# Performance work log

Measured on AMD Instinct MI355X. Metric: run time of the kernel, lower is better.

## Reference

```python
import jax, jax.numpy as jnp
import numpy as np

EPS = 1e-5
NUM_SUBSET = 3

def conv1x1(x, w, b):
    # x: (N,C,T,V), w: (O,C), b: (O,)
    return jnp.einsum('nctv,oc->notv', x, w) + b[None, :, None, None]

def batchnorm(x, w, b):
    m = x.mean(axis=(0, 2, 3), keepdims=True)
    v = x.var(axis=(0, 2, 3), keepdims=True)
    return (x - m) * jax.lax.rsqrt(v + EPS) * w[None, :, None, None] + b[None, :, None, None]

def setup_inputs() -> dict:
    key = jax.random.key(0)
    ks = jax.random.split(key, 16)
    N, C, T, V, R, O, S = 32, 64, 256, 25, 8, 64, NUM_SUBSET
    sc = 0.05
    return {
        'x1': jax.random.normal(ks[0], (N, C, T, V), jnp.float32),
        'x2': jax.random.normal(ks[1], (N, C, T, V), jnp.float32),
        'PA': jax.random.normal(ks[2], (S, V, V), jnp.float32) * sc,
        'alpha': jnp.zeros((1,), jnp.float32),
        'c1w': jax.random.normal(ks[3], (S, R, C), jnp.float32) * sc,
        'c1b': jnp.zeros((S, R), jnp.float32),
        'c2w': jax.random.normal(ks[4], (S, R, C), jnp.float32) * sc,
        'c2b': jnp.zeros((S, R), jnp.float32),
        'c3w': jax.random.normal(ks[5], (S, O, C), jnp.float32) * sc,
        'c3b': jnp.zeros((S, O), jnp.float32),
        'c4w': jax.random.normal(ks[6], (S, O, C), jnp.float32) * sc,
        'c4b': jnp.zeros((S, O), jnp.float32),
        'c5w': jax.random.normal(ks[7], (S, O, R), jnp.float32) * sc,
        'c5b': jnp.zeros((S, O), jnp.float32),
        'c6w': jax.random.normal(ks[8], (S, O, R), jnp.float32) * sc,
        'c6b': jnp.zeros((S, O), jnp.float32),
        'bn1_w': jax.random.uniform(ks[9], (O,), jnp.float32),
        'bn1_b': jnp.zeros((O,), jnp.float32),
        'bn2_w': jax.random.uniform(ks[10], (O,), jnp.float32),
        'bn2_b': jnp.zeros((O,), jnp.float32),
    }

def reference(x1, x2, PA, alpha, c1w, c1b, c2w, c2b, c3w, c3b, c4w, c4b,
              c5w, c5b, c6w, c6b, bn1_w, bn1_b, bn2_w, bn2_b):
    y1 = y2 = None
    for i in range(NUM_SUBSET):
        r1 = conv1x1(x1, c1w[i], c1b[i]).mean(axis=2)  # (N,R,V)
        r2 = conv1x1(x2, c2w[i], c2b[i]).mean(axis=2)  # (N,R,V)
        x3 = conv1x1(x1, c3w[i], c3b[i])               # (N,O,T,V)
        x4 = conv1x1(x2, c4w[i], c4b[i])               # (N,O,T,V)
        rel = jnp.tanh(r1[:, :, :, None] - r2[:, :, None, :])  # (N,R,V,V)
        # NOTE: source passes self.alpha (scalar param) into the A2 slot,
        # so the `alpha` multiplier on conv5 defaults to 1.
        a1 = jnp.einsum('nruv,or->nouv', rel, c5w[i]) + c5b[i][None, :, None, None]
        a1 = a1 + PA[i][None, None, :, :]
        a2 = jnp.einsum('nruv,or->nouv', rel, c6w[i]) + c6b[i][None, :, None, None] + alpha
        z1 = jnp.einsum('ncuv,nctv->nctu', a1, x3)
        z2 = jnp.einsum('ncuv,nctv->nctu', a2, x4)
        y1 = z1 if y1 is None else y1 + z1
        y2 = z2 if y2 is None else y2 + z2
    # in_channels == out_channels -> residual down is identity
    y1 = jax.nn.relu(batchnorm(y1, bn1_w, bn1_b) + x1)
    y2 = jax.nn.relu(batchnorm(y2, bn2_w, bn2_b) + x2)
    return (y1, y2)
```

## Files before the change

### kernel.cpp

```cpp
#include <hip/hip_runtime.h>

typedef float  f32x4  __attribute__((ext_vector_type(4)));
typedef short  bf16x8 __attribute__((ext_vector_type(8)));
typedef short  s16x4  __attribute__((ext_vector_type(4)));

__device__ __forceinline__ unsigned short f2bf(float f) {
    unsigned int u = __float_as_uint(f);
    unsigned int r = (u + 0x7FFFu + ((u >> 16) & 1u)) >> 16;
    return (unsigned short)r;
}
__device__ __forceinline__ float bf2f(unsigned short h) {
    return __uint_as_float(((unsigned int)h) << 16);
}

__global__ __launch_bounds__(256) void kT_transpose(
    const float* __restrict__ x1, const float* __restrict__ x2,
    float* __restrict__ xm, unsigned short* __restrict__ xT)
{
    const int tc = blockIdx.x, n = blockIdx.y, p = blockIdx.z;
    const float* __restrict__ x = p ? x2 : x1;
    __shared__ unsigned short tile[64 * 225];
    const int tid = threadIdx.x;

    const size_t xb = (size_t)n * 409600 + (size_t)tc * 200;
    for (int k = 0; k < 13; k++) {
        const int idx = tid + k * 256;
        if (idx < 3200) {
            const int c = idx / 50, l = idx % 50;
            const f32x4 v = *(const f32x4*)(x + xb + (size_t)c * 6400 + l * 4);
            const int base = c * 225 + l * 4;
            tile[base + 0] = f2bf(v[0]);
            tile[base + 1] = f2bf(v[1]);
            tile[base + 2] = f2bf(v[2]);
            tile[base + 3] = f2bf(v[3]);
        }
    }
    __syncthreads();

    for (int k = 0; k < 7; k++) {
        const int idx = tid + k * 256;
        if (idx < 1600) {
            const int c = idx / 25, v = idx % 25;
            float s = 0.f;
            #pragma unroll
            for (int t = 0; t < 8; t++) s += bf2f(tile[c * 225 + t * 25 + v]);
            atomicAdd(&xm[((size_t)(p * 32 + n) * 64 + c) * 25 + v],
                      s * (1.0f / 256.0f));
        }
    }

    for (int k = 0; k < 7; k++) {
        const int idx = tid + k * 256;
        if (idx < 1600) {
            const int c8 = idx & 7, pos = idx >> 3;
            bf16x8 o;
            #pragma unroll
            for (int j = 0; j < 8; j++)
                o[j] = (short)tile[(c8 * 8 + j) * 225 + pos];
            *(bf16x8*)(xT + (((size_t)(p * 32 + n) * 6400 + tc * 200 + pos) * 64
                             + c8 * 8)) = o;
        }
    }
}

__global__ void k2_adj(const float* __restrict__ xm,
                       const float* __restrict__ PA, const float* __restrict__ alpha,
                       const float* __restrict__ c1w, const float* __restrict__ c1b,
                       const float* __restrict__ c2w, const float* __restrict__ c2b,
                       const float* __restrict__ c5w, const float* __restrict__ c5b,
                       const float* __restrict__ c6w, const float* __restrict__ c6b,
                       unsigned short* __restrict__ aw,
                       const float* __restrict__ c3w, const float* __restrict__ c4w,
                       unsigned short* __restrict__ awW)
{
    const int b = blockIdx.x;
    const int tid = threadIdx.x;

    if (b >= 192) {
        const int pi = b - 192;
        const int p = pi / 3, i = pi % 3;
        const int cg = tid >> 6, lane = tid & 63, q = lane >> 4, m = lane & 15;
        const float* w3 = p ? c4w : c3w;
        const float* wr = w3 + (size_t)(i * 64 + cg * 16 + m) * 64 + q * 8;
        const f32x4 w00 = *(const f32x4*)(wr);
        const f32x4 w01 = *(const f32x4*)(wr + 4);
        const f32x4 w10 = *(const f32x4*)(wr + 32);
        const f32x4 w11 = *(const f32x4*)(wr + 36);
        bf16x8 af0, af1;
        #pragma unroll
        for (int k = 0; k < 4; k++) {
            af0[k] = (short)f2bf(w00[k]); af0[k + 4] = (short)f2bf(w01[k]);
            af1[k] = (short)f2bf(w10[k]); af1[k + 4] = (short)f2bf(w11[k]);
        }
        unsigned short* o = awW + ((size_t)(pi * 4 + cg) * 64 + lane) * 16;
        *(bf16x8*)(o)     = af0;
        *(bf16x8*)(o + 8) = af1;
        return;
    }

    const int i = b >> 6;
    const int n = (b >> 1) & 31;
    const int pp = b & 1;
    __shared__ float xml[3200];
    __shared__ float rl[400];
    __shared__ float rel[5000];

    for (int idx = tid; idx < 3200; idx += 256) {
        const int p_ = idx / 1600, rest = idx % 1600;
        xml[idx] = xm[(size_t)(p_ * 32 + n) * 1600 + rest];
    }
    __syncthreads();

    for (int idx = tid; idx < 400; idx += 256) {
        const int which = idx / 200;
        const int rr = (idx % 200) / 25;
        const int v = idx % 25;
        const float* wv = (which ? c2w : c1w) + (i * 8 + rr) * 64;
        const float* xp = xml + which * 1600;
        float s = (which ? c2b : c1b)[i * 8 + rr];
        for (int c = 0; c < 64; c++) s += wv[c] * xp[c * 25 + v];
        rl[idx] = s;
    }
    __syncthreads();

    for (int idx = tid; idx < 5000; idx += 256) {
        const int r_ = idx / 625;
        const int rem = idx - r_ * 625;
        const int u = rem / 25;
        const int v = rem - u * 25;
        rel[idx] = tanhf(rl[r_ * 25 + u] - rl[200 + r_ * 25 + v]);
    }
    __syncthreads();

    const float al = alpha[0];
    {
        const int p_ = pp;
        const float* w5 = p_ ? c6w : c5w;
        const float* b5 = p_ ? c6b : c5b;
        for (int idx = tid; idx < 8192; idx += 256) {
            const int c = idx >> 7;
            const int ut = (idx >> 6) & 1;
            const int lane = idx & 63;
            const int u = ut * 16 + (lane & 15);
            const int qd = lane >> 4;
            bf16x8 outv;
            if (u < 25) {
                float wrow[8];
                #pragma unroll
                for (int r = 0; r < 8; r++) wrow[r] = w5[(i * 64 + c) * 8 + r];
                const float bias = b5[i * 64 + c];
                #pragma unroll
                for (int j = 0; j < 8; j++) {
                    const int v = qd * 8 + j;
                    float s = 0.f;
                    if (v < 25) {
                        s = bias + (p_ ? al : PA[i * 625 + u * 25 + v]);
                        #pragma unroll
                        for (int r = 0; r < 8; r++) s += rel[r * 625 + u * 25 + v] * wrow[r];
                    }
                    outv[j] = (short)f2bf(s);
                }
            } else {
                #pragma unroll
                for (int j = 0; j < 8; j++) outv[j] = 0;
            }
            *(bf16x8*)(aw + ((size_t)((p_ * 3 + i) * 32 + n) * 64 + c) * 1024
                          + ut * 512 + lane * 8) = outv;
        }
    }
}

__global__ __launch_bounds__(256, 3) void kF_main(
    const unsigned short* __restrict__ xT,
    const float* __restrict__ c3b, const float* __restrict__ c4b,
    const unsigned short* __restrict__ awW,
    const unsigned short* __restrict__ aw,
    unsigned short* __restrict__ z,
    float* __restrict__ ppart)
{
    const int flat = blockIdx.x;
    const int lidx = flat >> 3;
    const int grp  = (flat & 7) * 8 + (lidx >> 6);
    const int within = lidx & 63;
    const int tc = within & 15, cg = within >> 4;
    const int n = grp & 31, p = grp >> 5;

    __shared__ unsigned short X3s[2][16 * 512];
    const int tid = threadIdx.x, w = tid >> 6, lane = tid & 63;
    const int q = lane >> 4, m = lane & 15;

    {
        int* xi = (int*)&X3s[0][0];
        #pragma unroll
        for (int k = 0; k < 32; k++) xi[tid + k * 256] = 0;
    }

    const float* __restrict__ b3 = p ? c4b : c3b;
    const size_t xTb = ((size_t)(p * 32 + n) * 6400 + (size_t)tc * 400) * 64;

    bf16x8 xr0[7], xr1[7];
    #pragma unroll
    for (int k = 0; k < 7; k++) {
        const int g = w + 4 * k;
        if (g < 25) {
            const unsigned short* xp = xT + xTb + (size_t)(g * 16 + m) * 64 + q * 8;
            xr0[k] = *(const bf16x8*)(xp);
            xr1[k] = *(const bf16x8*)(xp + 32);
        }
    }

    f32x4 acc[4][2];
    #pragma unroll
    for (int a = 0; a < 4; a++) {
        acc[a][0] = (f32x4){0.f, 0.f, 0.f, 0.f};
        acc[a][1] = (f32x4){0.f, 0.f, 0.f, 0.f};
    }

    __syncthreads();

    for (int i = 0; i < 3; i++) {
        bf16x8 B0[4], B1[4];
        #pragma unroll
        for (int cl4 = 0; cl4 < 4; cl4++) {
            const int c = cg * 16 + w * 4 + cl4;
            const unsigned short* ab =
                aw + ((size_t)((p * 3 + i) * 32 + n) * 64 + c) * 1024 + lane * 8;
            B0[cl4] = *(const bf16x8*)(ab);
            B1[cl4] = *(const bf16x8*)(ab + 512);
        }

        const unsigned short* wp =
            awW + ((size_t)((p * 3 + i) * 4 + cg) * 64 + lane) * 16;
        const bf16x8 af0 = *(const bf16x8*)(wp);
        const bf16x8 af1 = *(const bf16x8*)(wp + 8);
        float bb[4];
        #pragma unroll
        for (int r = 0; r < 4; r++) bb[r] = b3[i * 64 + cg * 16 + q * 4 + r];

        unsigned short* Xb = &X3s[i & 1][0];
        #pragma unroll
        for (int k = 0; k < 7; k++) {
            const int g = w + 4 * k;
            if (g < 25) {
                f32x4 d = (f32x4){0.f, 0.f, 0.f, 0.f};
                d = __builtin_amdgcn_mfma_f32_16x16x32_bf16(af0, xr0[k], d, 0, 0, 0);
                d = __builtin_amdgcn_mfma_f32_16x16x32_bf16(af1, xr1[k], d, 0, 0, 0);
                const int pos = g * 16 + m;
                const int t = pos / 25, v = pos - t * 25;
                #pragma unroll
                for (int r = 0; r < 4; r++)
                    Xb[(q * 4 + r) * 512 + t * 32 + v] = f2bf(d[r] + bb[r]);
            }
        }
        __syncthreads();

        #pragma unroll
        for (int cl4 = 0; cl4 < 4; cl4++) {
            const int cl = w * 4 + cl4;
            const bf16x8 A = *(const bf16x8*)(Xb + cl * 512 + m * 32 + q * 8);
            acc[cl4][0] = __builtin_amdgcn_mfma_f32_16x16x32_bf16(A, B0[cl4], acc[cl4][0], 0, 0, 0);
            acc[cl4][1] = __builtin_amdgcn_mfma_f32_16x16x32_bf16(A, B1[cl4], acc[cl4][1], 0, 0, 0);
        }
    }
    __syncthreads();

    unsigned short* stg = &X3s[0][0];
    #pragma unroll
    for (int cl4 = 0; cl4 < 4; cl4++) {
        float sum = 0.f, ssq = 0.f;
        #pragma unroll
        for (int r = 0; r < 4; r++) {
            const float v0 = acc[cl4][0][r];
            sum += v0; ssq += v0 * v0;
        }
        if (m < 9) {
            #pragma unroll
            for (int r = 0; r < 4; r++) {
                const float v1 = acc[cl4][1][r];
                sum += v1; ssq += v1 * v1;
            }
        }
        #pragma unroll
        for (int off = 32; off > 0; off >>= 1) {
            sum += __shfl_xor(sum, off, 64);
            ssq += __shfl_xor(ssq, off, 64);
        }
        const int c = cg * 16 + w * 4 + cl4;
        if (lane == 0) {
            float* pp = ppart + ((size_t)(p * 64 + c) * 512 + n * 16 + tc) * 2;
            pp[0] = sum; pp[1] = ssq;
        }
        #pragma unroll
        for (int ut = 0; ut < 2; ut++) {
            if (ut == 0 || m < 9) {
                #pragma unroll
                for (int r = 0; r < 4; r++)
                    stg[w * 1600 + cl4 * 400 + (q * 4 + r) * 25 + ut * 16 + m] =
                        f2bf(acc[cl4][ut][r]);
            }
        }
    }
    for (int rd = 0; rd < 4; rd++) {
        const int idx = rd * 64 + lane;
        if (idx < 200) {
            const int cl4 = idx / 50, oct = idx % 50;
            const bf16x8 vz = *(const bf16x8*)(stg + w * 1600 + cl4 * 400 + oct * 8);
            const int c = cg * 16 + w * 4 + cl4;
            *(bf16x8*)(z + ((size_t)((p * 32 + n) * 64 + c)) * 6400
                         + tc * 400 + oct * 8) = vz;
        }
    }
}

__global__ void k4_finalize(const float* __restrict__ ppart,
                            const float* __restrict__ bn1w, const float* __restrict__ bn1b,
                            const float* __restrict__ bn2w, const float* __restrict__ bn2b,
                            float* __restrict__ ss)
{
    const int b = blockIdx.x;
    const int t = threadIdx.x;
    const float* base = ppart + (size_t)b * 1024;
    float s = 0.f, qs = 0.f;
    #pragma unroll
    for (int k = 0; k < 8; k++) {
        const int idx = t + 64 * k;
        s  += base[idx * 2];
        qs += base[idx * 2 + 1];
    }
    #pragma unroll
    for (int off = 32; off > 0; off >>= 1) {
        s  += __shfl_xor(s,  off, 64);
        qs += __shfl_xor(qs, off, 64);
    }
    if (t == 0) {
        const int p = b >> 6, c = b & 63;
        const float cnt = 204800.f;
        const float mean = s / cnt;
        const float var  = qs / cnt - mean * mean;
        const float gw = p ? bn2w[c] : bn1w[c];
        const float gb = p ? bn2b[c] : bn1b[c];
        const float scale = gw * rsqrtf(var + 1e-5f);
        ss[b * 2]     = scale;
        ss[b * 2 + 1] = gb - mean * scale;
    }
}

__global__ __launch_bounds__(256) void k5_apply(
    const float* __restrict__ x1, const float* __restrict__ x2,
    const unsigned short* __restrict__ z, const float* __restrict__ ss,
    float* __restrict__ out)
{
    const unsigned int g = blockIdx.x * 256u + threadIdx.x;
    const unsigned int e = g * 4u;
    const int p = (e >= 13107200u) ? 1 : 0;
    const unsigned int c = (e / 6400u) & 63u;
    const float* xsrc = p ? x2 : x1;
    const f32x4 xv = *(const f32x4*)(xsrc + (e - (unsigned int)p * 13107200u));
    const s16x4 zv = *(const s16x4*)(const void*)(z + e);
    const float scale = ss[(p * 64 + c) * 2];
    const float shift = ss[(p * 64 + c) * 2 + 1];
    f32x4 o;
    #pragma unroll
    for (int k = 0; k < 4; k++) {
        const float zf = bf2f((unsigned short)zv[k]);
        const float y = zf * scale + shift + xv[k];
        o[k] = y > 0.f ? y : 0.f;
    }
    *(f32x4*)(out + e) = o;
}

extern "C" void kernel_launch(void* const* d_in, const int* in_sizes, int n_in,
                              void* d_out, int out_size, void* d_ws, size_t ws_size,
                              hipStream_t stream)
{
    (void)in_sizes; (void)n_in; (void)out_size; (void)ws_size;
    const float* x1   = (const float*)d_in[0];
    const float* x2   = (const float*)d_in[1];
    const float* PA   = (const float*)d_in[2];
    const float* alp  = (const float*)d_in[3];
    const float* c1w  = (const float*)d_in[4];
    const float* c1b  = (const float*)d_in[5];
    const float* c2w  = (const float*)d_in[6];
    const float* c2b  = (const float*)d_in[7];
    const float* c3w  = (const float*)d_in[8];
    const float* c3b  = (const float*)d_in[9];
    const float* c4w  = (const float*)d_in[10];
    const float* c4b  = (const float*)d_in[11];
    const float* c5w  = (const float*)d_in[12];
    const float* c5b  = (const float*)d_in[13];
    const float* c6w  = (const float*)d_in[14];
    const float* c6b  = (const float*)d_in[15];
    const float* bn1w = (const float*)d_in[16];
    const float* bn1b = (const float*)d_in[17];
    const float* bn2w = (const float*)d_in[18];
    const float* bn2b = (const float*)d_in[19];

    char* ws = (char*)d_ws;
    float*          xm    = (float*)(ws + 0);
    unsigned short* aw    = (unsigned short*)(ws + 409600);
    unsigned short* xT    = (unsigned short*)(ws + 25575424);
    unsigned short* zbuf  = (unsigned short*)(ws + 78004224);
    float*          ppart = (float*)(ws + 130433024);
    float*          ss    = (float*)(ws + 130957312);
    unsigned short* awW   = (unsigned short*)(ws + 130958336);

    hipMemsetAsync(xm, 0, 409600, stream);

    kT_transpose<<<dim3(32, 32, 2), 256, 0, stream>>>(x1, x2, xm, xT);
    k2_adj<<<198, 256, 0, stream>>>(xm, PA, alp, c1w, c1b, c2w, c2b,
                                    c5w, c5b, c6w, c6b, aw, c3w, c4w, awW);
    kF_main<<<dim3(4096), 256, 0, stream>>>(xT, c3b, c4b, awW, aw,
                                            zbuf, ppart);
    k4_finalize<<<128, 64, 0, stream>>>(ppart, bn1w, bn1b, bn2w, bn2b, ss);
    k5_apply<<<25600, 256, 0, stream>>>(x1, x2, zbuf, ss, (float*)d_out);
}
```

Baseline: 373.8 us.

## Pipeline kF stages with swizzled LDS, replace atomics with partial means

Several changes at once. The time-mean now goes to per-tile partial buffers that k2 sums, replacing the atomics and the memset. kF_main is software-pipelined so stage-1 MFMA for subset i+1 overlaps stage-2 for subset i, with one fewer barrier per iteration. LDS tiles get an XOR swizzle and padding to cut bank conflicts. Float-to-bf16 conversion uses the packed hip intrinsic. This adds register pressure in kF and extra reads in k2, and the partial buffer aliases zbuf.

```diff
diff --git a/kernel.cpp b/kernel.cpp
--- a/kernel.cpp
+++ b/kernel.cpp
@@ -1,13 +1,17 @@
 #include <hip/hip_runtime.h>
+#include <hip/hip_bf16.h>
 
 typedef float  f32x4  __attribute__((ext_vector_type(4)));
 typedef short  bf16x8 __attribute__((ext_vector_type(8)));
 typedef short  s16x4  __attribute__((ext_vector_type(4)));
 
 __device__ __forceinline__ unsigned short f2bf(float f) {
-    unsigned int u = __float_as_uint(f);
-    unsigned int r = (u + 0x7FFFu + ((u >> 16) & 1u)) >> 16;
-    return (unsigned short)r;
+    __hip_bfloat16 h = __float2bfloat16(f);
+    return *reinterpret_cast<unsigned short*>(&h);
+}
+__device__ __forceinline__ unsigned int f2bf2(float a, float b) {
+    __hip_bfloat162 h = __float22bfloat162_rn(make_float2(a, b));
+    return *reinterpret_cast<unsigned int*>(&h);
 }
 __device__ __forceinline__ float bf2f(unsigned short h) {
     return __uint_as_float(((unsigned int)h) << 16);
@@ -15,11 +19,11 @@
 
 __global__ __launch_bounds__(256) void kT_transpose(
     const float* __restrict__ x1, const float* __restrict__ x2,
-    float* __restrict__ xm, unsigned short* __restrict__ xT)
+    float* __restrict__ xmp, unsigned short* __restrict__ xT)
 {
     const int tc = blockIdx.x, n = blockIdx.y, p = blockIdx.z;
     const float* __restrict__ x = p ? x2 : x1;
-    __shared__ unsigned short tile[64 * 225];
+    __shared__ unsigned short tile[64 * 226];
     const int tid = threadIdx.x;
 
     const size_t xb = (size_t)n * 409600 + (size_t)tc * 200;
@@ -28,11 +32,9 @@
         if (idx < 3200) {
             const int c = idx / 50, l = idx % 50;
             const f32x4 v = *(const f32x4*)(x + xb + (size_t)c * 6400 + l * 4);
-            const int base = c * 225 + l * 4;
-            tile[base + 0] = f2bf(v[0]);
-            tile[base + 1] = f2bf(v[1]);
-            tile[base + 2] = f2bf(v[2]);
-            tile[base + 3] = f2bf(v[3]);
+            unsigned int* dst = (unsigned int*)&tile[c * 226 + l * 4];
+            dst[0] = f2bf2(v[0], v[1]);
+            dst[1] = f2bf2(v[2], v[3]);
         }
     }
     __syncthreads();
@@ -43,9 +45,9 @@
             const int c = idx / 25, v = idx % 25;
             float s = 0.f;
             #pragma unroll
-            for (int t = 0; t < 8; t++) s += bf2f(tile[c * 225 + t * 25 + v]);
-            atomicAdd(&xm[((size_t)(p * 32 + n) * 64 + c) * 25 + v],
-                      s * (1.0f / 256.0f));
+            for (int t = 0; t < 8; t++) s += bf2f(tile[c * 226 + t * 25 + v]);
+            xmp[((size_t)((p * 32 + n) * 32 + tc)) * 1600 + idx] =
+                s * (1.0f / 256.0f);
         }
     }
 
@@ -56,14 +58,14 @@
             bf16x8 o;
             #pragma unroll
             for (int j = 0; j < 8; j++)
-                o[j] = (short)tile[(c8 * 8 + j) * 225 + pos];
+                o[j] = (short)tile[(c8 * 8 + j) * 226 + pos];
             *(bf16x8*)(xT + (((size_t)(p * 32 + n) * 6400 + tc * 200 + pos) * 64
                              + c8 * 8)) = o;
         }
     }
 }
 
-__global__ void k2_adj(const float* __restrict__ xm,
+__global__ void k2_adj(const float* __restrict__ xmp,
                        const float* __restrict__ PA, const float* __restrict__ alpha,
                        const float* __restrict__ c1w, const float* __restrict__ c1b,
                        const float* __restrict__ c2w, const float* __restrict__ c2b,
@@ -105,9 +107,13 @@
     __shared__ float rl[400];
     __shared__ float rel[5000];
 
-    for (int idx = tid; idx < 3200; idx += 256) {
-        const int p_ = idx / 1600, rest = idx % 1600;
-        xml[idx] = xm[(size_t)(p_ * 32 + n) * 1600 + rest];
+    for (int idx = tid; idx < 800; idx += 256) {
+        const int p_ = idx / 400, r4 = (idx % 400) * 4;
+        f32x4 s = (f32x4){0.f, 0.f, 0.f, 0.f};
+        #pragma unroll 4
+        for (int tcc = 0; tcc < 32; tcc++)
+            s += *(const f32x4*)(xmp + ((size_t)((p_ * 32 + n) * 32 + tcc)) * 1600 + r4);
+        *(f32x4*)(xml + p_ * 1600 + r4) = s;
     }
     __syncthreads();
 
@@ -170,6 +176,53 @@
     }
 }
 
+#define KF_STAGE1(I, BUF)                                                     \
+    {                                                                         \
+        const unsigned short* wp =                                            \
+            awW + ((size_t)((p * 3 + (I)) * 4 + cg) * 64 + lane) * 16;        \
+        const bf16x8 af0 = *(const bf16x8*)(wp);                              \
+        const bf16x8 af1 = *(const bf16x8*)(wp + 8);                          \
+        float bb[4];                                                          \
+        _Pragma("unroll")                                                     \
+        for (int r = 0; r < 4; r++) bb[r] = b3[(I) * 64 + cg * 16 + q * 4 + r]; \
+        _Pragma("unroll")                                                     \
+        for (int k = 0; k < 7; k++) {                                         \
+            const int g = w + 4 * k;                                          \
+            if (g < 25) {                                                     \
+                f32x4 d = (f32x4){0.f, 0.f, 0.f, 0.f};                        \
+                d = __builtin_amdgcn_mfma_f32_16x16x32_bf16(af0, xr0[k], d, 0, 0, 0); \
+                d = __builtin_amdgcn_mfma_f32_16x16x32_bf16(af1, xr1[k], d, 0, 0, 0); \
+                const int pos = g * 16 + m;                                   \
+                const int t = pos / 25, v = pos - t * 25;                     \
+                const int key = ((t >> 1) & 3) << 3;                          \
+                _Pragma("unroll")                                             \
+                for (int r = 0; r < 4; r++)                                   \
+                    X3s[BUF][(q * 4 + r) * 512 + t * 32 + (v ^ key)] =        \
+                        f2bf(d[r] + bb[r]);                                   \
+            }                                                                 \
+        }                                                                     \
+    }
+
+#define KF_LOADB(I)                                                           \
+    _Pragma("unroll")                                                         \
+    for (int cl4 = 0; cl4 < 4; cl4++) {                                       \
+        const int c = cg * 16 + w * 4 + cl4;                                  \
+        const unsigned short* ab =                                            \
+            aw + ((size_t)((p * 3 + (I)) * 32 + n) * 64 + c) * 1024 + lane * 8; \
+        B0[cl4] = *(const bf16x8*)(ab);                                       \
+        B1[cl4] = *(const bf16x8*)(ab + 512);                                 \
+    }
+
+#define KF_STAGE2(BUF)                                                        \
+    _Pragma("unroll")                                                         \
+    for (int cl4 = 0; cl4 < 4; cl4++) {                                       \
+        const int cl = w * 4 + cl4;                                           \
+        const bf16x8 A = *(const bf16x8*)(                                    \
+            &X3s[BUF][cl * 512 + m * 32 + ((q * 8) ^ (((m >> 1) & 3) << 3))]); \
+        acc[cl4][0] = __builtin_amdgcn_mfma_f32_16x16x32_bf16(A, B0[cl4], acc[cl4][0], 0, 0, 0); \
+        acc[cl4][1] = __builtin_amdgcn_mfma_f32_16x16x32_bf16(A, B1[cl4], acc[cl4][1], 0, 0, 0); \
+    }
+
 __global__ __launch_bounds__(256, 3) void kF_main(
     const unsigned short* __restrict__ xT,
     const float* __restrict__ c3b, const float* __restrict__ c4b,
@@ -185,7 +238,7 @@
     const int tc = within & 15, cg = within >> 4;
     const int n = grp & 31, p = grp >> 5;
 
-    __shared__ unsigned short X3s[2][16 * 512];
+    __shared__ unsigned short X3s[2][8192];
     const int tid = threadIdx.x, w = tid >> 6, lane = tid & 63;
     const int q = lane >> 4, m = lane & 15;
 
@@ -218,53 +271,29 @@
 
     __syncthreads();
 
-    for (int i = 0; i < 3; i++) {
+    KF_STAGE1(0, 0);
+    __syncthreads();
+    {
         bf16x8 B0[4], B1[4];
-        #pragma unroll
-        for (int cl4 = 0; cl4 < 4; cl4++) {
-            const int c = cg * 16 + w * 4 + cl4;
-            const unsigned short* ab =
-                aw + ((size_t)((p * 3 + i) * 32 + n) * 64 + c) * 1024 + lane * 8;
-            B0[cl4] = *(const bf16x8*)(ab);
-            B1[cl4] = *(const bf16x8*)(ab + 512);
-        }
-
-        const unsigned short* wp =
-            awW + ((size_t)((p * 3 + i) * 4 + cg) * 64 + lane) * 16;
-        const bf16x8 af0 = *(const bf16x8*)(wp);
-        const bf16x8 af1 = *(const bf16x8*)(wp + 8);
-        float bb[4];
-        #pragma unroll
-        for (int r = 0; r < 4; r++) bb[r] = b3[i * 64 + cg * 16 + q * 4 + r];
-
-        unsigned short* Xb = &X3s[i & 1][0];
-        #pragma unroll
-        for (int k = 0; k < 7; k++) {
-            const int g = w + 4 * k;
-            if (g < 25) {
-                f32x4 d = (f32x4){0.f, 0.f, 0.f, 0.f};
-                d = __builtin_amdgcn_mfma_f32_16x16x32_bf16(af0, xr0[k], d, 0, 0, 0);
-                d = __builtin_amdgcn_mfma_f32_16x16x32_bf16(af1, xr1[k], d, 0, 0, 0);
-                const int pos = g * 16 + m;
-                const int t = pos / 25, v = pos - t * 25;
-                #pragma unroll
-                for (int r = 0; r < 4; r++)
-                    Xb[(q * 4 + r) * 512 + t * 32 + v] = f2bf(d[r] + bb[r]);
-            }
-        }
-        __syncthreads();
-
-        #pragma unroll
-        for (int cl4 = 0; cl4 < 4; cl4++) {
-            const int cl = w * 4 + cl4;
-            const bf16x8 A = *(const bf16x8*)(Xb + cl * 512 + m * 32 + q * 8);
-            acc[cl4][0] = __builtin_amdgcn_mfma_f32_16x16x32_bf16(A, B0[cl4], acc[cl4][0], 0, 0, 0);
-            acc[cl4][1] = __builtin_amdgcn_mfma_f32_16x16x32_bf16(A, B1[cl4], acc[cl4][1], 0, 0, 0);
-        }
-    }
-    __syncthreads();
-
-    unsigned short* stg = &X3s[0][0];
+        KF_LOADB(0);
+        KF_STAGE1(1, 1);
+        KF_STAGE2(0);
+    }
+    __syncthreads();
+    {
+        bf16x8 B0[4], B1[4];
+        KF_LOADB(1);
+        KF_STAGE1(2, 0);
+        KF_STAGE2(1);
+    }
+    __syncthreads();
+    {
+        bf16x8 B0[4], B1[4];
+        KF_LOADB(2);
+        KF_STAGE2(0);
+    }
+
+    unsigned short* stg = &X3s[1][0];
     #pragma unroll
     for (int cl4 = 0; cl4 < 4; cl4++) {
         float sum = 0.f, ssq = 0.f;
@@ -396,18 +425,16 @@
     const float* bn2b = (const float*)d_in[19];
 
     char* ws = (char*)d_ws;
-    float*          xm    = (float*)(ws + 0);
-    unsigned short* aw    = (unsigned short*)(ws + 409600);
-    unsigned short* xT    = (unsigned short*)(ws + 25575424);
-    unsigned short* zbuf  = (unsigned short*)(ws + 78004224);
-    float*          ppart = (float*)(ws + 130433024);
-    float*          ss    = (float*)(ws + 130957312);
-    unsigned short* awW   = (unsigned short*)(ws + 130958336);
-
-    hipMemsetAsync(xm, 0, 409600, stream);
-
-    kT_transpose<<<dim3(32, 32, 2), 256, 0, stream>>>(x1, x2, xm, xT);
-    k2_adj<<<198, 256, 0, stream>>>(xm, PA, alp, c1w, c1b, c2w, c2b,
+    unsigned short* aw    = (unsigned short*)(ws + 0);
+    unsigned short* xT    = (unsigned short*)(ws + 25165824);
+    unsigned short* zbuf  = (unsigned short*)(ws + 77594624);
+    float*          ppart = (float*)(ws + 130023424);
+    float*          ss    = (float*)(ws + 130547712);
+    unsigned short* awW   = (unsigned short*)(ws + 130548736);
+    float*          xmp   = (float*)zbuf;
+
+    kT_transpose<<<dim3(32, 32, 2), 256, 0, stream>>>(x1, x2, xmp, xT);
+    k2_adj<<<198, 256, 0, stream>>>(xmp, PA, alp, c1w, c1b, c2w, c2b,
                                     c5w, c5b, c6w, c6b, aw, c3w, c4w, awW);
     kF_main<<<dim3(4096), 256, 0, stream>>>(xT, c3b, c4b, awW, aw,
                                             zbuf, ppart);
```

After: 379.1 us. Within noise of the previous version (+1.4%).
